# Optimization experiments

Hardware: AMD Instinct MI355X
Metric: run time of the kernel (lower is better)

The kernel has to match this reference:

```python
import jax, jax.numpy as jnp
import numpy as np

NH, NKV, D = 16, 8, 128
HID = 2048
EPS = 1e-6
ROPE_BASE = 10000.0
T = 2048


def setup_inputs() -> dict:
    key = jax.random.key(0)
    k1, k2, k3 = jax.random.split(key, 3)
    return {
        "positions": jnp.arange(T, dtype=jnp.int32),
        "hidden_states": jax.random.normal(k1, (T, HID), dtype=jnp.float32),
        "w_qkv": jax.random.normal(k2, (HID, (NH + 2 * NKV) * D), dtype=jnp.float32) * 0.02,
        "w_o": jax.random.normal(k3, (NH * D, HID), dtype=jnp.float32) * 0.02,
        "q_norm_w": jnp.ones((D,), dtype=jnp.float32),
        "k_norm_w": jnp.ones((D,), dtype=jnp.float32),
    }


def _rmsnorm(x, w):
    # per-head RMSNorm over last dim (head_dim)
    return x * jax.lax.rsqrt(jnp.mean(x * x, axis=-1, keepdims=True) + EPS) * w


def reference(positions, hidden_states, w_qkv, w_o, q_norm_w, k_norm_w):
    t = hidden_states.shape[0]
    scale = D ** -0.5

    # fused QKV projection, then split
    qkv = hidden_states @ w_qkv                       # [T, (NH+2*NKV)*D]
    q, k, v = jnp.split(qkv, [NH * D, (NH + NKV) * D], axis=-1)
    q = q.reshape(t, NH, D)
    k = k.reshape(t, NKV, D)
    v = v.reshape(t, NKV, D)

    # per-head QK RMSNorm (Qwen3)
    q = _rmsnorm(q, q_norm_w)
    k = _rmsnorm(k, k_norm_w)

    # RoPE (neox style: rotate half-split pairs)
    inv_freq = 1.0 / (ROPE_BASE ** (jnp.arange(0, D, 2, dtype=jnp.float32) / D))
    freqs = positions.astype(jnp.float32)[:, None] * inv_freq  # [T, D/2]
    cos = jnp.cos(freqs)[:, None, :]                   # [T, 1, D/2]
    sin = jnp.sin(freqs)[:, None, :]

    def rope(x):
        x1, x2 = jnp.split(x, 2, axis=-1)
        return jnp.concatenate([x1 * cos - x2 * sin, x2 * cos + x1 * sin], axis=-1)

    q = rope(q)
    k = rope(k)

    # GQA: repeat kv heads
    g = NH // NKV
    kr = jnp.repeat(k, g, axis=1)                      # [T, NH, D]
    vr = jnp.repeat(v, g, axis=1)

    # causal attention
    scores = jnp.einsum('thd,shd->hts', q, kr) * scale  # [NH, T, T]
    causal = jnp.tril(jnp.ones((t, t), dtype=bool))
    scores = jnp.where(causal[None], scores, -jnp.inf)
    probs = jax.nn.softmax(scores, axis=-1)
    o = jnp.einsum('hts,shd->thd', probs, vr).reshape(t, NH * D)

    return o @ w_o
```

## Files before the change

### kernel.cpp

```cpp
#include <hip/hip_runtime.h>
#include <math.h>

#define T_TOK 2048
#define HIDDEN 2048
#define NH 16
#define NKV 8
#define DH 128

typedef unsigned short u16;
typedef __attribute__((ext_vector_type(8))) short bf16x8;
typedef __attribute__((ext_vector_type(4))) float f32x4;

__device__ __forceinline__ u16 f2bf(float f) {
  union { float f; unsigned u; } x; x.f = f;
  unsigned r = (x.u + 0x7fffu + ((x.u >> 16) & 1u)) >> 16;
  return (u16)r;
}

__device__ __forceinline__ float bf2f(u16 v) {
  union { unsigned u; float f; } x; x.u = ((unsigned)v) << 16;
  return x.f;
}

__device__ __forceinline__ void gload16(const void* g, void* l) {
  __builtin_amdgcn_global_load_lds((const __attribute__((address_space(1))) void*)g,
                                   (__attribute__((address_space(3))) void*)l,
                                   16, 0, 0);
}

__global__ __launch_bounds__(256) void prepass(const float* __restrict__ hidden,
                                               const float* __restrict__ w_qkv,
                                               const float* __restrict__ w_o,
                                               u16* __restrict__ Xb,
                                               u16* __restrict__ WqkvT,
                                               u16* __restrict__ WoT) {
  __shared__ float tile[64][65];
  const int b = blockIdx.x;
  if (b < 4096) {
    int i = b * 256 + threadIdx.x;
    float4 v = ((const float4*)hidden)[i];
    ushort4 o;
    o.x = f2bf(v.x); o.y = f2bf(v.y); o.z = f2bf(v.z); o.w = f2bf(v.w);
    ((ushort4*)Xb)[i] = o;
    return;
  }
  const float* in; u16* out; int R, Cdim, c0, r0;
  if (b < 6144) {
    int bb = b - 4096;
    in = w_qkv; out = WqkvT; R = 2048; Cdim = 4096;
    c0 = (bb & 63) * 64; r0 = (bb >> 6) * 64;
  } else {
    int bb = b - 6144;
    in = w_o; out = WoT; R = 2048; Cdim = 2048;
    c0 = (bb & 31) * 64; r0 = (bb >> 5) * 64;
  }
  const int tx = threadIdx.x & 63, ty = threadIdx.x >> 6;
#pragma unroll
  for (int i = 0; i < 64; i += 4)
    tile[ty + i][tx] = in[(size_t)(r0 + ty + i) * Cdim + c0 + tx];
  __syncthreads();
#pragma unroll
  for (int i = 0; i < 64; i += 4)
    out[(size_t)(c0 + ty + i) * R + r0 + tx] = f2bf(tile[tx][ty + i]);
}

__global__ __launch_bounds__(256) void add_parts4(const u16* __restrict__ a,
                                                  const u16* __restrict__ b,
                                                  const u16* __restrict__ c,
                                                  const u16* __restrict__ d,
                                                  float* __restrict__ o, int n4) {
  int i = blockIdx.x * blockDim.x + threadIdx.x;
  if (i < n4) {
    ushort4 x = ((const ushort4*)a)[i], y = ((const ushort4*)b)[i];
    ushort4 u = ((const ushort4*)c)[i], v = ((const ushort4*)d)[i];
    float4 z;
    z.x = bf2f(x.x) + bf2f(y.x) + bf2f(u.x) + bf2f(v.x);
    z.y = bf2f(x.y) + bf2f(y.y) + bf2f(u.y) + bf2f(v.y);
    z.z = bf2f(x.z) + bf2f(y.z) + bf2f(u.z) + bf2f(v.z);
    z.w = bf2f(x.w) + bf2f(y.w) + bf2f(u.w) + bf2f(v.w);
    ((float4*)o)[i] = z;
  }
}

__global__ __launch_bounds__(256) void rope_vt(const u16* __restrict__ qkv0,
                                               const u16* __restrict__ qkv1,
                                               const int* __restrict__ pos,
                                               const float* __restrict__ qw,
                                               const float* __restrict__ kw,
                                               u16* __restrict__ Qg,
                                               u16* __restrict__ Kg,
                                               u16* __restrict__ Vt,
                                               unsigned* __restrict__ counter) {
  __shared__ float tile[64][65];
  const int b = blockIdx.x;
  if (b < 12288) {
    const int wave = threadIdx.x >> 6, j = threadIdx.x & 63;
    const int idx = b * 4 + wave;
    const int t = idx & 2047, slot = idx >> 11;
    const float QSC = 0.088388347648318447f * 1.4426950408889634f;
    const size_t base_i = (size_t)t * 4096 + slot * 128;
    float x1 = bf2f(qkv0[base_i + j]) + bf2f(qkv1[base_i + j]);
    float x2 = bf2f(qkv0[base_i + j + 64]) + bf2f(qkv1[base_i + j + 64]);
    float ss = x1 * x1 + x2 * x2;
#pragma unroll
    for (int m = 1; m < 64; m <<= 1) ss += __shfl_xor(ss, m);
    float r = rsqrtf(ss * (1.0f / 128.0f) + 1e-6f);
    const bool isq = slot < NH;
    const float* w = isq ? qw : kw;
    float xn1 = x1 * r * w[j], xn2 = x2 * r * w[j + 64];
    float fp = (float)pos[t];
    float inv_freq = exp2f(-(float)j * (13.287712379549449f / 64.0f));
    float ang = fp * inv_freq;
    float sn, cs;
    sincosf(ang, &sn, &cs);
    float o1 = xn1 * cs - xn2 * sn;
    float o2 = xn2 * cs + xn1 * sn;
    if (isq) {
      size_t base = ((size_t)slot * T_TOK + t) * DH;
      Qg[base + j] = f2bf(o1 * QSC); Qg[base + 64 + j] = f2bf(o2 * QSC);
    } else {
      size_t base = ((size_t)(slot - NH) * T_TOK + t) * DH;
      Kg[base + j] = f2bf(o1); Kg[base + 64 + j] = f2bf(o2);
    }
    return;
  }
  if (b == 12288 && threadIdx.x == 0) *counter = 0u;
  const int bb = b - 12288;
  const int h = bb & 7, rest = bb >> 3;
  const int t0 = (rest & 31) * 64, d0 = (rest >> 5) * 64;
  const int tx = threadIdx.x & 63, ty = threadIdx.x >> 6;
#pragma unroll
  for (int i = 0; i < 64; i += 4) {
    size_t gi = (size_t)(t0 + ty + i) * 4096 + (NH + NKV) * DH + h * DH + d0 + tx;
    tile[ty + i][tx] = bf2f(qkv0[gi]) + bf2f(qkv1[gi]);
  }
  __syncthreads();
#pragma unroll
  for (int i = 0; i < 64; i += 4)
    Vt[((size_t)h * DH + d0 + ty + i) * T_TOK + t0 + tx] = f2bf(tile[tx][ty + i]);
}

__global__ __launch_bounds__(512, 2) void gemm256(const u16* __restrict__ A,
                                                  const u16* __restrict__ Bt,
                                                  void* __restrict__ Cout,
                                                  int M, int N, int K, int lda, int ldb,
                                                  int obf16) {
  __shared__ __attribute__((aligned(128))) char lds[131072];

  const int nx = N >> 8, ny = M >> 8;
  const int flat = blockIdx.x;
  const int per = gridDim.x >> 3;
  const int swz = (flat & 7) * per + (flat >> 3);
  const int by = swz % ny;
  const int rest = swz / ny;
  const int bx = rest % nx;
  const int bz = rest / nx;
  const int m0 = by << 8, n0 = bx << 8;
  A += (size_t)bz * K;
  Bt += (size_t)bz * K;

  const int tid = threadIdx.x;
  const int wave = tid >> 6, lane = tid & 63;
  const int l15 = lane & 15, quad = lane >> 4;
  const int wr = wave >> 2, wc = wave & 3;

  size_t aoff[2], boff[2];
#pragma unroll
  for (int c = 0; c < 2; ++c) {
    int chunk = c * 512 + tid;
    int line = chunk >> 3;
    int ls8 = (chunk & 7) ^ (line & 7);
    int row = line * 2 + (ls8 >> 2);
    int ks = ls8 & 3;
    aoff[c] = (size_t)(m0 + row) * lda + ks * 8;
    boff[c] = (size_t)(n0 + row) * ldb + ks * 8;
  }

#define STAGE(tt) do {                                                  \
    char* db = lds + ((tt) & 3) * 16384 + wave * 1024;                  \
    const int kk = (tt) * 32;                                           \
    gload16(A + aoff[0] + kk, db);                                      \
    gload16(A + aoff[1] + kk, db + 8192);                               \
    gload16(Bt + boff[0] + kk, db + 65536);                             \
    gload16(Bt + boff[1] + kk, db + 65536 + 8192);                      \
  } while (0)

  const int fragoff = (l15 >> 1) * 128 +
                      (((((l15 & 1) << 2) | quad) ^ ((l15 >> 1) & 7)) << 4);

  const f32x4 zero = {0.f, 0.f, 0.f, 0.f};
  f32x4 acc[8][4];
#pragma unroll
  for (int i = 0; i < 8; ++i)
#pragma unroll
    for (int j = 0; j < 4; ++j) acc[i][j] = zero;

  const int NT = K >> 5;
  STAGE(0); STAGE(1); STAGE(2);
  asm volatile("s_waitcnt vmcnt(8)" ::: "memory");
  __builtin_amdgcn_s_barrier();

  for (int t = 0; t < NT; ++t) {
    const char* As = lds + (t & 3) * 16384 + wr * 8192 + fragoff;
    const char* Bs = lds + 65536 + (t & 3) * 16384 + wc * 4096 + fragoff;
    bf16x8 af[8], bfr[4];
#pragma unroll
    for (int mt = 0; mt < 8; ++mt) af[mt] = *(const bf16x8*)(As + mt * 1024);
#pragma unroll
    for (int nt = 0; nt < 4; ++nt) bfr[nt] = *(const bf16x8*)(Bs + nt * 1024);

    if (t + 3 < NT) STAGE(t + 3);

    __builtin_amdgcn_s_setprio(1);
#pragma unroll
    for (int mt = 0; mt < 8; ++mt)
#pragma unroll
      for (int nt = 0; nt < 4; ++nt)
        acc[mt][nt] = __builtin_amdgcn_mfma_f32_16x16x32_bf16(af[mt], bfr[nt], acc[mt][nt], 0, 0, 0);
    __builtin_amdgcn_s_setprio(0);

    const int rem = NT - 1 - t;
    if (rem >= 3)      asm volatile("s_waitcnt vmcnt(8)" ::: "memory");
    else if (rem == 2) asm volatile("s_waitcnt vmcnt(4)" ::: "memory");
    else if (rem == 1) asm volatile("s_waitcnt vmcnt(0)" ::: "memory");
    if (rem > 0) __builtin_amdgcn_s_barrier();
  }
#undef STAGE

  if (obf16) {
    u16* C = (u16*)Cout + (size_t)bz * M * N;
#pragma unroll
    for (int mt = 0; mt < 8; ++mt)
#pragma unroll
      for (int nt = 0; nt < 4; ++nt)
#pragma unroll
        for (int r = 0; r < 4; ++r)
          C[(size_t)(m0 + wr * 128 + mt * 16 + quad * 4 + r) * N + n0 + wc * 64 + nt * 16 + l15] =
              f2bf(acc[mt][nt][r]);
  } else {
    float* C = (float*)Cout + (size_t)bz * M * N;
#pragma unroll
    for (int mt = 0; mt < 8; ++mt)
#pragma unroll
      for (int nt = 0; nt < 4; ++nt)
#pragma unroll
        for (int r = 0; r < 4; ++r)
          C[(size_t)(m0 + wr * 128 + mt * 16 + quad * 4 + r) * N + n0 + wc * 64 + nt * 16 + l15] =
              acc[mt][nt][r];
  }
}

__global__ __launch_bounds__(256) void attn_kernel(const u16* __restrict__ Qg,
                                                   const u16* __restrict__ Kg,
                                                   const u16* __restrict__ Vtg,
                                                   float* __restrict__ Opart,
                                                   float* __restrict__ Lpart,
                                                   unsigned* __restrict__ counter) {
  __shared__ u16 Klds[2][64 * 128];
  __shared__ u16 Vlds[2][128 * 64];
  __shared__ u16 Plds[4][16 * 72];
  __shared__ unsigned item_s;
  const int wave = threadIdx.x >> 6, lane = threadIdx.x & 63;
  const int l15 = lane & 15, quad = lane >> 4;
  u16* Pw = &Plds[wave][0];
  const f32x4 zero = {0.f, 0.f, 0.f, 0.f};
  const float4 zero4 = {0.f, 0.f, 0.f, 0.f};

#define STAGEKV(jj, sl) do {                                            \
    u16* Kd = &Klds[sl][0]; u16* Vd = &Vlds[sl][0];                     \
    _Pragma("unroll")                                                   \
    for (int c = 0; c < 4; ++c) {                                       \
      int chunk = wave * 4 + c;                                         \
      int sL = chunk * 64 + lane;                                       \
      { int ss = sL >> 4;                                               \
        int g = (sL & 15) ^ (ss & 15);                                  \
        gload16(Kh + ((size_t)((jj) * 64 + ss)) * DH + g * 8, Kd + chunk * 512); } \
      { int d = sL >> 3;                                                \
        int g = (sL & 7) ^ (d & 7);                                     \
        gload16(Vh + (size_t)d * T_TOK + (jj) * 64 + g * 8, Vd + chunk * 512); } \
    } } while (0)

  for (;;) {
    __syncthreads();
    if (threadIdx.x == 0) item_s = atomicAdd(counter, 1u);
    __syncthreads();
    const unsigned item = item_s;
    if (item >= 1024u) break;
    const int qt = 31 - (int)(item >> 5);
    const int s  = (int)(item >> 4) & 1;
    const int h  = (int)item & 15;
    const int kvh = h >> 1;
    const int slot = (h * 32 + qt) * 2 + s;
    const int j0 = s ? (qt + 2) >> 1 : 0;
    const int j1 = s ? qt + 1 : (qt + 2) >> 1;

    float* Oslot = Opart + (size_t)slot * (64 * 128);

    if (j0 >= j1) {
      for (int t = threadIdx.x; t < 64 * 128 / 4; t += 256) ((float4*)Oslot)[t] = zero4;
      if (threadIdx.x < 64) Lpart[slot * 64 + threadIdx.x] = 0.f;
      continue;
    }

    const u16* Qh = Qg + (size_t)h * T_TOK * DH;
    const u16* Kh = Kg + (size_t)kvh * T_TOK * DH;
    const u16* Vh = Vtg + (size_t)kvh * DH * T_TOK;
    const int qrow0 = qt * 64 + wave * 16;

    bf16x8 qf[4];
#pragma unroll
    for (int ks = 0; ks < 4; ++ks)
      qf[ks] = *(const bf16x8*)(Qh + (size_t)(qrow0 + l15) * DH + ks * 32 + quad * 8);

    f32x4 oacc[8];
#pragma unroll
    for (int i = 0; i < 8; ++i) oacc[i] = zero;
    float l_i[4] = {0.f, 0.f, 0.f, 0.f};

    STAGEKV(j0, 0);
    asm volatile("s_waitcnt vmcnt(0)" ::: "memory");
    __builtin_amdgcn_s_barrier();

    for (int j = j0; j < j1; ++j) {
      const int sl = (j - j0) & 1;
      if (j + 1 < j1) STAGEKV(j + 1, sl ^ 1);
      const u16* Kl = &Klds[sl][0];
      const u16* Vl = &Vlds[sl][0];

      f32x4 sacc[4];
#pragma unroll
      for (int nt = 0; nt < 4; ++nt) sacc[nt] = zero;
      __builtin_amdgcn_s_setprio(1);
#pragma unroll
      for (int nt = 0; nt < 4; ++nt) {
        int sr = nt * 16 + l15;
#pragma unroll
        for (int ks = 0; ks < 4; ++ks) {
          bf16x8 kf = *(const bf16x8*)&Kl[sr * 128 + (((ks * 4 + quad) ^ (sr & 15)) * 8)];
          sacc[nt] = __builtin_amdgcn_mfma_f32_16x16x32_bf16(qf[ks], kf, sacc[nt], 0, 0, 0);
        }
      }
      __builtin_amdgcn_s_setprio(0);

      if (j == qt) {
#pragma unroll
        for (int nt = 0; nt < 4; ++nt)
#pragma unroll
          for (int r = 0; r < 4; ++r) {
            int col = j * 64 + nt * 16 + l15;
            int row = qrow0 + quad * 4 + r;
            if (col > row) sacc[nt][r] = -INFINITY;
          }
      }

#pragma unroll
      for (int nt = 0; nt < 4; ++nt)
#pragma unroll
        for (int r = 0; r < 4; ++r) {
          float pv = exp2f(sacc[nt][r]);
          unsigned u = __float_as_uint(pv);
          Pw[(quad * 4 + r) * 72 + nt * 16 + l15] = (u16)(u >> 16);
          l_i[r] += __uint_as_float(u & 0xffff0000u);
        }

      bf16x8 pf[2];
#pragma unroll
      for (int ks = 0; ks < 2; ++ks)
        pf[ks] = *(const bf16x8*)&Pw[l15 * 72 + ks * 32 + quad * 8];
      __builtin_amdgcn_s_setprio(1);
#pragma unroll
      for (int ot = 0; ot < 8; ++ot) {
        int d = ot * 16 + l15;
#pragma unroll
        for (int ks = 0; ks < 2; ++ks) {
          bf16x8 vf = *(const bf16x8*)&Vl[d * 64 + (((ks * 4 + quad) ^ (d & 7)) * 8)];
          oacc[ot] = __builtin_amdgcn_mfma_f32_16x16x32_bf16(pf[ks], vf, oacc[ot], 0, 0, 0);
        }
      }
      __builtin_amdgcn_s_setprio(0);

      if (j + 1 < j1) {
        asm volatile("s_waitcnt vmcnt(0)" ::: "memory");
        __builtin_amdgcn_s_barrier();
      }
    }

#pragma unroll
    for (int ot = 0; ot < 8; ++ot)
#pragma unroll
      for (int r = 0; r < 4; ++r)
        Oslot[(wave * 16 + quad * 4 + r) * 128 + ot * 16 + l15] = oacc[ot][r];
#pragma unroll
    for (int msk = 1; msk < 16; msk <<= 1)
#pragma unroll
      for (int r = 0; r < 4; ++r) l_i[r] += __shfl_xor(l_i[r], msk);
    if (l15 == 0) {
#pragma unroll
      for (int r = 0; r < 4; ++r)
        Lpart[slot * 64 + wave * 16 + quad * 4 + r] = l_i[r];
    }
  }
#undef STAGEKV
}

__global__ __launch_bounds__(256) void attn_merge(const float* __restrict__ Opart,
                                                  const float* __restrict__ Lpart,
                                                  u16* __restrict__ Og) {
  const int b = blockIdx.x;
  const int h = b & 15, qt = b >> 4;
  const int slot0 = (h * 32 + qt) * 2, slot1 = slot0 + 1;
  const float4* O0 = (const float4*)(Opart + (size_t)slot0 * (64 * 128));
  const float4* O1 = (const float4*)(Opart + (size_t)slot1 * (64 * 128));
#pragma unroll
  for (int it = 0; it < 8; ++it) {
    int idx = it * 256 + threadIdx.x;
    int r = idx >> 5, c4 = idx & 31;
    float rl = 1.0f / (Lpart[slot0 * 64 + r] + Lpart[slot1 * 64 + r]);
    float4 a = O0[idx], c = O1[idx];
    int row = qt * 64 + r, col = c4 * 4;
    u16* dst = Og + (size_t)row * (NH * DH) + h * DH + col;
    dst[0] = f2bf((a.x + c.x) * rl);
    dst[1] = f2bf((a.y + c.y) * rl);
    dst[2] = f2bf((a.z + c.z) * rl);
    dst[3] = f2bf((a.w + c.w) * rl);
  }
}

extern "C" void kernel_launch(void* const* d_in, const int* in_sizes, int n_in,
                              void* d_out, int out_size, void* d_ws, size_t ws_size,
                              hipStream_t stream) {
  (void)in_sizes; (void)n_in; (void)out_size; (void)ws_size;
  const int* positions = (const int*)d_in[0];
  const float* hidden  = (const float*)d_in[1];
  const float* w_qkv   = (const float*)d_in[2];
  const float* w_o     = (const float*)d_in[3];
  const float* q_norm  = (const float*)d_in[4];
  const float* k_norm  = (const float*)d_in[5];
  float* out = (float*)d_out;

  char* ws = (char*)d_ws;
  u16*   Xb    = (u16*)(ws);
  u16*   WqkvT = (u16*)(ws + ( 8ull << 20));
  u16*   WoT   = (u16*)(ws + (24ull << 20));
  u16*   P0    = (u16*)(ws + (32ull << 20));
  u16*   P1    = P0 + (size_t)T_TOK * 4096;
  u16*   Qg    = (u16*)(ws + (64ull << 20));
  u16*   Kg    = (u16*)(ws + (72ull << 20));
  u16*   Vt    = (u16*)(ws + (76ull << 20));
  u16*   AttnO = (u16*)(ws + (80ull << 20));
  float* Opart = (float*)(ws + (32ull << 20));
  float* Lpart = (float*)(ws);
  unsigned* ctr = (unsigned*)(ws + (512ull << 10));
  u16*   G2P   = (u16*)(ws + (32ull << 20));

  prepass<<<dim3(7168), 256, 0, stream>>>(hidden, w_qkv, w_o, Xb, WqkvT, WoT);

  gemm256<<<dim3(256), 512, 0, stream>>>(
      Xb, WqkvT, P0, T_TOK, 4096, 1024, HIDDEN, HIDDEN, 1);

  rope_vt<<<dim3(12288 + 512), 256, 0, stream>>>(P0, P1, positions,
                                                 q_norm, k_norm, Qg, Kg, Vt, ctr);

  attn_kernel<<<dim3(512), 256, 0, stream>>>(Qg, Kg, Vt, Opart, Lpart, ctr);
  attn_merge<<<dim3(512), 256, 0, stream>>>(Opart, Lpart, AttnO);

  gemm256<<<dim3(256), 512, 0, stream>>>(
      AttnO, WoT, G2P, T_TOK, HIDDEN, 512, NH * DH, NH * DH, 1);
  const int n4 = T_TOK * HIDDEN / 4;
  add_parts4<<<dim3(n4 / 256), 256, 0, stream>>>(
      G2P, G2P + (size_t)T_TOK * HIDDEN, G2P + 2 * (size_t)T_TOK * HIDDEN,
      G2P + 3 * (size_t)T_TOK * HIDDEN, out, n4);
}
```

Baseline: 247.4 us.

## Use 128x256 GEMM tiles and cut split-K partitions for both projections

Replaces the 256x256 GEMM tile with a 128x256 tile, using smaller LDS and accumulator arrays. The QKV projection no longer uses split-K, so rope_vt reads one bf16 buffer instead of summing two partials. The output projection goes from 4 split-K partitions to 2, which reduces partial-buffer traffic in the final add kernel. Each block now does longer K loops with less A reuse per tile, and the Q/K/Vt workspace buffers are moved to new offsets.

```diff
diff --git a/kernel.cpp b/kernel.cpp
--- a/kernel.cpp
+++ b/kernel.cpp
@@ -64,26 +64,22 @@
     out[(size_t)(c0 + ty + i) * R + r0 + tx] = f2bf(tile[tx][ty + i]);
 }
 
-__global__ __launch_bounds__(256) void add_parts4(const u16* __restrict__ a,
+__global__ __launch_bounds__(256) void add_parts2(const u16* __restrict__ a,
                                                   const u16* __restrict__ b,
-                                                  const u16* __restrict__ c,
-                                                  const u16* __restrict__ d,
                                                   float* __restrict__ o, int n4) {
   int i = blockIdx.x * blockDim.x + threadIdx.x;
   if (i < n4) {
     ushort4 x = ((const ushort4*)a)[i], y = ((const ushort4*)b)[i];
-    ushort4 u = ((const ushort4*)c)[i], v = ((const ushort4*)d)[i];
     float4 z;
-    z.x = bf2f(x.x) + bf2f(y.x) + bf2f(u.x) + bf2f(v.x);
-    z.y = bf2f(x.y) + bf2f(y.y) + bf2f(u.y) + bf2f(v.y);
-    z.z = bf2f(x.z) + bf2f(y.z) + bf2f(u.z) + bf2f(v.z);
-    z.w = bf2f(x.w) + bf2f(y.w) + bf2f(u.w) + bf2f(v.w);
+    z.x = bf2f(x.x) + bf2f(y.x);
+    z.y = bf2f(x.y) + bf2f(y.y);
+    z.z = bf2f(x.z) + bf2f(y.z);
+    z.w = bf2f(x.w) + bf2f(y.w);
     ((float4*)o)[i] = z;
   }
 }
 
-__global__ __launch_bounds__(256) void rope_vt(const u16* __restrict__ qkv0,
-                                               const u16* __restrict__ qkv1,
+__global__ __launch_bounds__(256) void rope_vt(const u16* __restrict__ qkv,
                                                const int* __restrict__ pos,
                                                const float* __restrict__ qw,
                                                const float* __restrict__ kw,
@@ -99,8 +95,8 @@
     const int t = idx & 2047, slot = idx >> 11;
     const float QSC = 0.088388347648318447f * 1.4426950408889634f;
     const size_t base_i = (size_t)t * 4096 + slot * 128;
-    float x1 = bf2f(qkv0[base_i + j]) + bf2f(qkv1[base_i + j]);
-    float x2 = bf2f(qkv0[base_i + j + 64]) + bf2f(qkv1[base_i + j + 64]);
+    float x1 = bf2f(qkv[base_i + j]);
+    float x2 = bf2f(qkv[base_i + j + 64]);
     float ss = x1 * x1 + x2 * x2;
 #pragma unroll
     for (int m = 1; m < 64; m <<= 1) ss += __shfl_xor(ss, m);
@@ -132,7 +128,7 @@
 #pragma unroll
   for (int i = 0; i < 64; i += 4) {
     size_t gi = (size_t)(t0 + ty + i) * 4096 + (NH + NKV) * DH + h * DH + d0 + tx;
-    tile[ty + i][tx] = bf2f(qkv0[gi]) + bf2f(qkv1[gi]);
+    tile[ty + i][tx] = bf2f(qkv[gi]);
   }
   __syncthreads();
 #pragma unroll
@@ -140,14 +136,14 @@
     Vt[((size_t)h * DH + d0 + ty + i) * T_TOK + t0 + tx] = f2bf(tile[tx][ty + i]);
 }
 
-__global__ __launch_bounds__(512, 2) void gemm256(const u16* __restrict__ A,
-                                                  const u16* __restrict__ Bt,
-                                                  void* __restrict__ Cout,
-                                                  int M, int N, int K, int lda, int ldb,
-                                                  int obf16) {
-  __shared__ __attribute__((aligned(128))) char lds[131072];
-
-  const int nx = N >> 8, ny = M >> 8;
+__global__ __launch_bounds__(512, 2) void gemm128x256(const u16* __restrict__ A,
+                                                      const u16* __restrict__ Bt,
+                                                      void* __restrict__ Cout,
+                                                      int M, int N, int K,
+                                                      int lda, int ldb, int obf16) {
+  __shared__ __attribute__((aligned(128))) char lds[98304];
+
+  const int nx = N >> 8, ny = M >> 7;
   const int flat = blockIdx.x;
   const int per = gridDim.x >> 3;
   const int swz = (flat & 7) * per + (flat >> 3);
@@ -155,7 +151,7 @@
   const int rest = swz / ny;
   const int bx = rest % nx;
   const int bz = rest / nx;
-  const int m0 = by << 8, n0 = bx << 8;
+  const int m0 = by << 7, n0 = bx << 8;
   A += (size_t)bz * K;
   Bt += (size_t)bz * K;
 
@@ -164,7 +160,16 @@
   const int l15 = lane & 15, quad = lane >> 4;
   const int wr = wave >> 2, wc = wave & 3;
 
-  size_t aoff[2], boff[2];
+  size_t aoff;
+  {
+    int chunk = tid;
+    int line = chunk >> 3;
+    int ls8 = (chunk & 7) ^ (line & 7);
+    int row = line * 2 + (ls8 >> 2);
+    int ks = ls8 & 3;
+    aoff = (size_t)(m0 + row) * lda + ks * 8;
+  }
+  size_t boff[2];
 #pragma unroll
   for (int c = 0; c < 2; ++c) {
     int chunk = c * 512 + tid;
@@ -172,40 +177,39 @@
     int ls8 = (chunk & 7) ^ (line & 7);
     int row = line * 2 + (ls8 >> 2);
     int ks = ls8 & 3;
-    aoff[c] = (size_t)(m0 + row) * lda + ks * 8;
     boff[c] = (size_t)(n0 + row) * ldb + ks * 8;
   }
 
-#define STAGE(tt) do {                                                  \
-    char* db = lds + ((tt) & 3) * 16384 + wave * 1024;                  \
-    const int kk = (tt) * 32;                                           \
-    gload16(A + aoff[0] + kk, db);                                      \
-    gload16(A + aoff[1] + kk, db + 8192);                               \
-    gload16(Bt + boff[0] + kk, db + 65536);                             \
-    gload16(Bt + boff[1] + kk, db + 65536 + 8192);                      \
+#define STAGE(tt) do {                                                   \
+    char* da = lds + ((tt) & 3) * 8192 + wave * 1024;                    \
+    char* db = lds + 32768 + ((tt) & 3) * 16384 + wave * 1024;           \
+    const int kk = (tt) * 32;                                            \
+    gload16(A + aoff + kk, da);                                          \
+    gload16(Bt + boff[0] + kk, db);                                      \
+    gload16(Bt + boff[1] + kk, db + 8192);                               \
   } while (0)
 
   const int fragoff = (l15 >> 1) * 128 +
                       (((((l15 & 1) << 2) | quad) ^ ((l15 >> 1) & 7)) << 4);
 
   const f32x4 zero = {0.f, 0.f, 0.f, 0.f};
-  f32x4 acc[8][4];
-#pragma unroll
-  for (int i = 0; i < 8; ++i)
+  f32x4 acc[4][4];
+#pragma unroll
+  for (int i = 0; i < 4; ++i)
 #pragma unroll
     for (int j = 0; j < 4; ++j) acc[i][j] = zero;
 
   const int NT = K >> 5;
   STAGE(0); STAGE(1); STAGE(2);
-  asm volatile("s_waitcnt vmcnt(8)" ::: "memory");
+  asm volatile("s_waitcnt vmcnt(6)" ::: "memory");
   __builtin_amdgcn_s_barrier();
 
   for (int t = 0; t < NT; ++t) {
-    const char* As = lds + (t & 3) * 16384 + wr * 8192 + fragoff;
-    const char* Bs = lds + 65536 + (t & 3) * 16384 + wc * 4096 + fragoff;
-    bf16x8 af[8], bfr[4];
-#pragma unroll
-    for (int mt = 0; mt < 8; ++mt) af[mt] = *(const bf16x8*)(As + mt * 1024);
+    const char* As = lds + (t & 3) * 8192 + wr * 4096 + fragoff;
+    const char* Bs = lds + 32768 + (t & 3) * 16384 + wc * 4096 + fragoff;
+    bf16x8 af[4], bfr[4];
+#pragma unroll
+    for (int mt = 0; mt < 4; ++mt) af[mt] = *(const bf16x8*)(As + mt * 1024);
 #pragma unroll
     for (int nt = 0; nt < 4; ++nt) bfr[nt] = *(const bf16x8*)(Bs + nt * 1024);
 
@@ -213,15 +217,15 @@
 
     __builtin_amdgcn_s_setprio(1);
 #pragma unroll
-    for (int mt = 0; mt < 8; ++mt)
+    for (int mt = 0; mt < 4; ++mt)
 #pragma unroll
       for (int nt = 0; nt < 4; ++nt)
         acc[mt][nt] = __builtin_amdgcn_mfma_f32_16x16x32_bf16(af[mt], bfr[nt], acc[mt][nt], 0, 0, 0);
     __builtin_amdgcn_s_setprio(0);
 
     const int rem = NT - 1 - t;
-    if (rem >= 3)      asm volatile("s_waitcnt vmcnt(8)" ::: "memory");
-    else if (rem == 2) asm volatile("s_waitcnt vmcnt(4)" ::: "memory");
+    if (rem >= 3)      asm volatile("s_waitcnt vmcnt(6)" ::: "memory");
+    else if (rem == 2) asm volatile("s_waitcnt vmcnt(3)" ::: "memory");
     else if (rem == 1) asm volatile("s_waitcnt vmcnt(0)" ::: "memory");
     if (rem > 0) __builtin_amdgcn_s_barrier();
   }
@@ -230,22 +234,22 @@
   if (obf16) {
     u16* C = (u16*)Cout + (size_t)bz * M * N;
 #pragma unroll
-    for (int mt = 0; mt < 8; ++mt)
+    for (int mt = 0; mt < 4; ++mt)
 #pragma unroll
       for (int nt = 0; nt < 4; ++nt)
 #pragma unroll
         for (int r = 0; r < 4; ++r)
-          C[(size_t)(m0 + wr * 128 + mt * 16 + quad * 4 + r) * N + n0 + wc * 64 + nt * 16 + l15] =
+          C[(size_t)(m0 + wr * 64 + mt * 16 + quad * 4 + r) * N + n0 + wc * 64 + nt * 16 + l15] =
               f2bf(acc[mt][nt][r]);
   } else {
     float* C = (float*)Cout + (size_t)bz * M * N;
 #pragma unroll
-    for (int mt = 0; mt < 8; ++mt)
+    for (int mt = 0; mt < 4; ++mt)
 #pragma unroll
       for (int nt = 0; nt < 4; ++nt)
 #pragma unroll
         for (int r = 0; r < 4; ++r)
-          C[(size_t)(m0 + wr * 128 + mt * 16 + quad * 4 + r) * N + n0 + wc * 64 + nt * 16 + l15] =
+          C[(size_t)(m0 + wr * 64 + mt * 16 + quad * 4 + r) * N + n0 + wc * 64 + nt * 16 + l15] =
               acc[mt][nt][r];
   }
 }
@@ -443,10 +447,9 @@
   u16*   WqkvT = (u16*)(ws + ( 8ull << 20));
   u16*   WoT   = (u16*)(ws + (24ull << 20));
   u16*   P0    = (u16*)(ws + (32ull << 20));
-  u16*   P1    = P0 + (size_t)T_TOK * 4096;
-  u16*   Qg    = (u16*)(ws + (64ull << 20));
-  u16*   Kg    = (u16*)(ws + (72ull << 20));
-  u16*   Vt    = (u16*)(ws + (76ull << 20));
+  u16*   Qg    = (u16*)(ws + ( 8ull << 20));
+  u16*   Kg    = (u16*)(ws + (16ull << 20));
+  u16*   Vt    = (u16*)(ws + (20ull << 20));
   u16*   AttnO = (u16*)(ws + (80ull << 20));
   float* Opart = (float*)(ws + (32ull << 20));
   float* Lpart = (float*)(ws);
@@ -455,19 +458,18 @@
 
   prepass<<<dim3(7168), 256, 0, stream>>>(hidden, w_qkv, w_o, Xb, WqkvT, WoT);
 
-  gemm256<<<dim3(256), 512, 0, stream>>>(
-      Xb, WqkvT, P0, T_TOK, 4096, 1024, HIDDEN, HIDDEN, 1);
-
-  rope_vt<<<dim3(12288 + 512), 256, 0, stream>>>(P0, P1, positions,
+  gemm128x256<<<dim3(256), 512, 0, stream>>>(
+      Xb, WqkvT, P0, T_TOK, 4096, HIDDEN, HIDDEN, HIDDEN, 1);
+
+  rope_vt<<<dim3(12288 + 512), 256, 0, stream>>>(P0, positions,
                                                  q_norm, k_norm, Qg, Kg, Vt, ctr);
 
   attn_kernel<<<dim3(512), 256, 0, stream>>>(Qg, Kg, Vt, Opart, Lpart, ctr);
   attn_merge<<<dim3(512), 256, 0, stream>>>(Opart, Lpart, AttnO);
 
-  gemm256<<<dim3(256), 512, 0, stream>>>(
-      AttnO, WoT, G2P, T_TOK, HIDDEN, 512, NH * DH, NH * DH, 1);
+  gemm128x256<<<dim3(256), 512, 0, stream>>>(
+      AttnO, WoT, G2P, T_TOK, HIDDEN, 1024, NH * DH, NH * DH, 1);
   const int n4 = T_TOK * HIDDEN / 4;
-  add_parts4<<<dim3(n4 / 256), 256, 0, stream>>>(
-      G2P, G2P + (size_t)T_TOK * HIDDEN, G2P + 2 * (size_t)T_TOK * HIDDEN,
-      G2P + 3 * (size_t)T_TOK * HIDDEN, out, n4);
-}
+  add_parts2<<<dim3(n4 / 256), 256, 0, stream>>>(
+      G2P, G2P + (size_t)T_TOK * HIDDEN, out, n4);
+}
```

Result: faster. 241.8 us (-2.3%).
